# Performance work log

Hardware: AMD Instinct MI355X
Metric: run time of the kernel (lower is better)

## Reference

```python
import jax, jax.numpy as jnp
import numpy as np

IN_CH = 64
NODE = 48
K_NEIGS = 10
KERNEL = 5
STRIDE = 2
BN_EPS = 1e-5


def _local_kernel(size, k, s):
    idx = np.arange(size * size).reshape(size, size)
    win = np.lib.stride_tricks.sliding_window_view(idx, (k, k))[::s, ::s]
    patches = win.reshape(-1, k * k)  # [n_edges, k*k] pixel indices
    n_edges = patches.shape[0]
    H = np.zeros((size * size, n_edges), dtype=np.float32)
    H[patches.reshape(-1), np.repeat(np.arange(n_edges), k * k)] = 1.0
    return jnp.asarray(H)


def _pairwise_distance(x):
    # (B,N,C) -> (B,N,N) squared euclidean
    xsq = jnp.sum(x * x, axis=-1, keepdims=True)
    return xsq - 2.0 * jnp.einsum('bnc,bmc->bnm', x, x) + jnp.swapaxes(xsq, 1, 2)


def _batched_knn(x, k):
    d = _pairwise_distance(x)
    avg = d.mean(-1, keepdims=True)
    neg_vals, inds = jax.lax.top_k(-d, k + 1)  # smallest k+1, sorted ascending
    return -neg_vals, inds, d, avg


def _incidence(inds, N):
    # weights_function(prob=False) == ones; scatter ones then transpose
    B, _, K = inds.shape
    b = jnp.arange(B)[:, None, None]
    p = jnp.arange(N)[None, :, None]
    M = jnp.zeros((B, N, N), dtype=jnp.float32).at[b, p, inds].set(1.0)
    return jnp.swapaxes(M, 1, 2)


def _generate_G(H):
    # G = diag(DV^-0.5) @ H @ I @ diag(DE^-1) @ H^T @ diag(DV^-0.5)
    DV = H.sum(axis=2)  # (B,N)
    DE = H.sum(axis=1)  # (B,E)
    dv2 = DV ** -0.5
    Hs = H * (1.0 / DE)[:, None, :]
    M = jnp.einsum('bne,bme->bnm', Hs, H)
    return dv2[:, :, None] * M * dv2[:, None, :]


def _build_G(x, local_H):
    B, N, C = x.shape
    _, topk_inds, _, _ = _batched_knn(x, K_NEIGS)
    H1 = _incidence(topk_inds, N)
    Dv = H1.sum(axis=2, keepdims=True)  # alpha = 1.0
    max_k = int(jnp.max(Dv))  # data-dependent width (eager, matches torch)
    _, ti2, _, _ = _batched_knn(x, max_k - 1)  # (B,N,max_k)
    tk = jnp.arange(max_k)[None, None, :]
    rng = jnp.broadcast_to(jnp.arange(N)[None, :, None], (B, N, max_k))
    new_inds = jnp.where(tk >= Dv, rng, ti2)
    new_H = _incidence(new_inds, N)
    loc = jnp.broadcast_to(local_H[None], (B,) + local_H.shape)
    return _generate_G(jnp.concatenate([new_H, loc], axis=2))


def _hgnn(x, G, W, b, gamma, beta):
    h = jnp.einsum('bnc,oc->bno', x, W) + b  # Linear
    h = jnp.einsum('bnm,bmc->bnc', G, h)
    mean = h.mean(axis=(0, 1))  # BatchNorm1d over (B,N) per channel
    var = h.var(axis=(0, 1))
    h = gamma * (h - mean) / jnp.sqrt(var + BN_EPS) + beta
    return jax.nn.relu(h) + x


def setup_inputs() -> dict:
    key = jax.random.key(0)
    k1, k2, k3 = jax.random.split(key, 3)
    B, N, C = 4, NODE * NODE, IN_CH
    x = jax.random.normal(k1, (B, N, C), dtype=jnp.float32)
    W = jax.random.normal(k2, (C, C), dtype=jnp.float32) / np.sqrt(C)
    b = jax.random.normal(k3, (C,), dtype=jnp.float32) * 0.01
    gamma = jnp.ones((C,), dtype=jnp.float32)
    beta = jnp.zeros((C,), dtype=jnp.float32)
    return {"x": x, "W": W, "b": b, "gamma": gamma, "beta": beta}


def reference(x, W, b, gamma, beta):
    local_H = _local_kernel(NODE, KERNEL, STRIDE)
    G = _build_G(x, local_H)  # graph construction is no_grad in torch
    return _hgnn(x, G, W, b, gamma, beta)
```

## Files before the change

### kernel.cpp

```cpp
#include <hip/hip_runtime.h>


#define HB    4
#define HN    2304
#define HC    64
#define HK    11
#define HL    48
#define HW    22
#define HE2   484
#define HE    (HN + HE2)
#define HRPB  4
#define NSLOT 36
#define NPAIRS (HB * HK * HN)

__global__ void hg14_sentinel(float* out, int n) {
    int i = blockIdx.x * 256 + threadIdx.x;
    if (i < n) out[i] = 12345.0f;
}

__global__ void hg14_init(int* Dv, int* indeg, float* bnsum, float* bnss) {
    int i = blockIdx.x * 256 + threadIdx.x;
    if (i < HB * HN) { Dv[i] = 0; indeg[i] = 0; }
    if (i < HC) { bnsum[i] = 0.f; bnss[i] = 0.f; }
}

__global__ __launch_bounds__(64) void hg14_linear(const float* x, const float* W,
                                                  const float* bias, float* h1,
                                                  float* xsq, float* xT) {
    int row = blockIdx.x;
    int t = threadIdx.x;
    __shared__ float xr[HC];
    float v = x[row * HC + t];
    xr[t] = v;
    __syncthreads();
    float sq = v * v;
    #pragma unroll
    for (int o = 32; o > 0; o >>= 1) sq += __shfl_xor(sq, o);
    if (t == 0) xsq[row] = sq;
    int b = row / HN, n = row % HN;
    xT[(b * HC + t) * HN + n] = v;
    float acc = bias[t];
    #pragma unroll 8
    for (int c = 0; c < HC; c++) acc += xr[c] * W[t * HC + c];
    h1[row * HC + t] = acc;
}

__device__ __forceinline__ unsigned hg14_wave_min_u32(unsigned v) {
    #pragma unroll
    for (int o = 32; o > 0; o >>= 1) {
        unsigned ov = __shfl_xor(v, o);
        v = ov < v ? ov : v;
    }
    return v;
}

#define HG14_INS4(q0, q1, q2, q3, x)                                     \
    {                                                                    \
        unsigned long long x_ = (x), n_;                                 \
        n_ = q0 < x_ ? q0 : x_; x_ = q0 < x_ ? x_ : q0; q0 = n_;         \
        n_ = q1 < x_ ? q1 : x_; x_ = q1 < x_ ? x_ : q1; q1 = n_;         \
        n_ = q2 < x_ ? q2 : x_; x_ = q2 < x_ ? x_ : q2; q2 = n_;         \
        if (x_ < q3) q3 = x_;                                            \
    }

#define HG14_CE(u, v)                                                    \
    { unsigned long long t_ = u < v ? u : v; v = u < v ? v : u; u = t_; }

#define HG14_BUILD()                                                               \
    {                                                                              \
        unsigned long long a0 = CINF, a1 = CINF, a2 = CINF, a3 = CINF;             \
        unsigned long long b0 = CINF, b1 = CINF, b2 = CINF, b3 = CINF;             \
        _Pragma("unroll")                                                          \
        for (int s = 0; s < NSLOT / 2; s++) {                                      \
            unsigned long long pa = ((unsigned long long)key[s] << 12) |           \
                                    (unsigned)((s << 6) | lane);                   \
            unsigned long long pb = ((unsigned long long)key[s + 18] << 12) |      \
                                    (unsigned)(((s + 18) << 6) | lane);            \
            HG14_INS4(a0, a1, a2, a3, pa);                                         \
            HG14_INS4(b0, b1, b2, b3, pb);                                         \
        }                                                                          \
        c0 = a0 < b3 ? a0 : b3; c1 = a1 < b2 ? a1 : b2;                            \
        c2 = a2 < b1 ? a2 : b1; c3 = a3 < b0 ? a3 : b0;                            \
        HG14_CE(c0, c2); HG14_CE(c1, c3); HG14_CE(c0, c1); HG14_CE(c2, c3);        \
    }

#define HG14_EXTRACT(kk, EMIT)                                                     \
    {                                                                              \
        for (int j = 0; j < (kk); j++) {                                           \
            unsigned hk = (unsigned)(c0 >> 12);                                    \
            unsigned mk = hg14_wave_min_u32(hk);                                   \
            unsigned long long bal = __ballot(hk == mk);                           \
            bool iswin;                                                            \
            if (__popcll(bal) == 1) {                                              \
                iswin = (hk == mk);                                                \
            } else {                                                               \
                unsigned mc = (hk == mk) ? (unsigned)(c0 & 0xFFFu) : 0xFFFFFFFFu;  \
                unsigned mm = hg14_wave_min_u32(mc);                               \
                iswin = (mc == mm);                                                \
            }                                                                      \
            if (iswin) {                                                           \
                int bi = (int)(c0 & 0xFFFu);                                       \
                EMIT;                                                              \
                unsigned long long popped = c0;                                    \
                c0 = c1; c1 = c2; c2 = c3; c3 = CINF;                              \
                if (c0 == CINF) {                                                  \
                    _Pragma("unroll")                                              \
                    for (int s = 0; s < NSLOT; s++) {                              \
                        unsigned long long pk =                                    \
                            ((unsigned long long)key[s] << 12) |                   \
                            (unsigned)((s << 6) | lane);                           \
                        if (pk > popped) HG14_INS4(c0, c1, c2, c3, pk);            \
                    }                                                              \
                }                                                                  \
            }                                                                      \
        }                                                                          \
    }

__device__ __forceinline__ void hg14_kth(const unsigned (&key)[NSLOT], int kk,
                                         unsigned& T, int& cntLess, int& take) {
    unsigned andv = 0xFFFFFFFFu, orv = 0u;
    #pragma unroll
    for (int s = 0; s < NSLOT; s++) { andv &= key[s]; orv |= key[s]; }
    #pragma unroll
    for (int o = 32; o > 0; o >>= 1) {
        andv &= (unsigned)__shfl_xor((int)andv, o);
        orv  |= (unsigned)__shfl_xor((int)orv, o);
    }
    unsigned diff = andv ^ orv;
    if (diff == 0u) { T = andv; cntLess = 0; take = kk; return; }
    int tstart = 31 - __builtin_clz(diff);
    unsigned lowmask = (tstart == 31) ? 0xFFFFFFFFu : ((1u << (tstart + 1)) - 1u);
    unsigned pref = andv & ~lowmask;
    int r = kk;
    for (int t = tstart; t >= 0; t--) {
        unsigned pt = pref >> t;
        int c = 0;
        #pragma unroll
        for (int s = 0; s < NSLOT; s++) c += ((key[s] >> t) == pt) ? 1 : 0;
        #pragma unroll
        for (int o = 32; o > 0; o >>= 1) c += __shfl_xor(c, o);
        if (r > c) { r -= c; pref |= (1u << t); }
    }
    T = pref; cntLess = kk - r; take = r;
}

__device__ __forceinline__ void hg14_scan64(int v, int lane, int& excl, int& total) {
    int inc = v;
    #pragma unroll
    for (int o = 1; o < 64; o <<= 1) {
        int u = __shfl_up(inc, o);
        if (lane >= o) inc += u;
    }
    excl = inc - v;
    total = __shfl(inc, 63);
}

__global__ __launch_bounds__(256) void hg14_knn_count(const float* xT, const float* xsq,
                                                      int* Dv, unsigned int* kcache,
                                                      int storekeys) {
    __shared__ float d[HRPB][HN];
    __shared__ __align__(16) float xrt[HC][HRPB];
    const int t = threadIdx.x;
    const int b = blockIdx.x / (HN / HRPB);
    const int n0 = (blockIdx.x % (HN / HRPB)) * HRPB;
    const int r = t >> 6;
    const int lane = t & 63;
    xrt[lane][r] = xT[(b * HC + lane) * HN + n0 + r];
    __syncthreads();
    float xs[HRPB];
    #pragma unroll
    for (int q = 0; q < HRPB; q++) xs[q] = xsq[b * HN + n0 + q];

    #pragma unroll
    for (int i = 0; i < 4; i++) {
        const int m = 512 * i + 2 * t;
        float2 d0 = {0.f, 0.f}, d1 = {0.f, 0.f}, d2 = {0.f, 0.f}, d3 = {0.f, 0.f};
        #pragma unroll 8
        for (int c = 0; c < HC; c++) {
            float4 xq = *reinterpret_cast<const float4*>(&xrt[c][0]);
            float2 xv = *reinterpret_cast<const float2*>(&xT[(b * HC + c) * HN + m]);
            d0.x += xq.x * xv.x; d0.y += xq.x * xv.y;
            d1.x += xq.y * xv.x; d1.y += xq.y * xv.y;
            d2.x += xq.z * xv.x; d2.y += xq.z * xv.y;
            d3.x += xq.w * xv.x; d3.y += xq.w * xv.y;
        }
        float s0 = xsq[b * HN + m], s1 = xsq[b * HN + m + 1];
        *reinterpret_cast<float2*>(&d[0][m]) =
            make_float2(xs[0] + s0 - 2.f * d0.x, xs[0] + s1 - 2.f * d0.y);
        *reinterpret_cast<float2*>(&d[1][m]) =
            make_float2(xs[1] + s0 - 2.f * d1.x, xs[1] + s1 - 2.f * d1.y);
        *reinterpret_cast<float2*>(&d[2][m]) =
            make_float2(xs[2] + s0 - 2.f * d2.x, xs[2] + s1 - 2.f * d2.y);
        *reinterpret_cast<float2*>(&d[3][m]) =
            make_float2(xs[3] + s0 - 2.f * d3.x, xs[3] + s1 - 2.f * d3.y);
    }
    {
        const int m = 2048 + t;
        float d0 = 0.f, d1 = 0.f, d2 = 0.f, d3 = 0.f;
        #pragma unroll 8
        for (int c = 0; c < HC; c++) {
            float4 xq = *reinterpret_cast<const float4*>(&xrt[c][0]);
            float xv = xT[(b * HC + c) * HN + m];
            d0 += xq.x * xv; d1 += xq.y * xv; d2 += xq.z * xv; d3 += xq.w * xv;
        }
        float sm = xsq[b * HN + m];
        d[0][m] = xs[0] + sm - 2.f * d0;
        d[1][m] = xs[1] + sm - 2.f * d1;
        d[2][m] = xs[2] + sm - 2.f * d2;
        d[3][m] = xs[3] + sm - 2.f * d3;
    }
    __syncthreads();

    const int p = n0 + r;
    const unsigned long long CINF = ~0ull;
    unsigned int key[NSLOT];
    unsigned long long c0, c1, c2, c3;
    const int rowbase = (b * HN + p) * NSLOT;
    #pragma unroll
    for (int s = 0; s < NSLOT; s++) {
        float f = d[r][(s << 6) | lane];
        unsigned int ub = __float_as_uint(f);
        unsigned int k = ub ^ (((unsigned int)(((int)ub) >> 31)) | 0x80000000u);
        key[s] = k;
        if (storekeys) kcache[(rowbase + s) * 64 + lane] = k;
    }
    HG14_BUILD();
    HG14_EXTRACT(HK, atomicAdd(&Dv[b * HN + bi], 1));
}

__global__ __launch_bounds__(256) void hg14_scan(const int* Dv, int* offs) {
    __shared__ int part[256];
    int t = threadIdx.x;
    int base = t * 36;
    int s = 0;
    for (int i = 0; i < 36; i++) s += max(Dv[base + i], 1);
    part[t] = s;
    __syncthreads();
    if (t == 0) { int acc = 0; for (int i = 0; i < 256; i++) { int v = part[i]; part[i] = acc; acc += v; } }
    __syncthreads();
    int acc = part[t];
    for (int i = 0; i < 36; i++) { offs[base + i] = acc; acc += max(Dv[base + i], 1); }
}

__device__ __forceinline__ void hg14_select_emit(const unsigned (&key)[NSLOT],
                                                 int b, int p, int lane, int kk, int base,
                                                 int* indeg, unsigned int* pairs) {
    unsigned T; int cntLess, take;
    hg14_kth(key, kk, T, cntLess, take);
    int cl = 0;
    #pragma unroll
    for (int s = 0; s < NSLOT; s++) cl += (key[s] < T) ? 1 : 0;
    int off, tot;
    hg14_scan64(cl, lane, off, tot);
    int w = 0;
    #pragma unroll
    for (int s = 0; s < NSLOT; s++) {
        if (key[s] < T) {
            int m = (s << 6) | lane;
            atomicAdd(&indeg[b * HN + m], 1);
            pairs[base + off + w] =
                ((unsigned)b << 24) | ((unsigned)p << 12) | (unsigned)m;
            w++;
        }
    }
    int lastm = -1;
    for (int t2 = 0; t2 < take; t2++) {
        int mc = 0x7FFFFFFF;
        #pragma unroll
        for (int s = 0; s < NSLOT; s++) {
            int m = (s << 6) | lane;
            if (key[s] == T && m > lastm && m < mc) mc = m;
        }
        int mmin = mc;
        #pragma unroll
        for (int o = 32; o > 0; o >>= 1) {
            int ov = __shfl_xor(mmin, o);
            mmin = ov < mmin ? ov : mmin;
        }
        if (mc == mmin) {
            atomicAdd(&indeg[b * HN + mmin], 1);
            pairs[base + cntLess + t2] =
                ((unsigned)b << 24) | ((unsigned)p << 12) | (unsigned)mmin;
        }
        lastm = mmin;
    }
}

__global__ __launch_bounds__(256) void hg14_knn_sel_cached(const unsigned int* kcache,
                                                           const int* Dv, const int* offs,
                                                           int* indeg, unsigned int* pairs) {
    const int t = threadIdx.x;
    const int lane = t & 63;
    const int gw = blockIdx.x * HRPB + (t >> 6);
    const int b = gw / HN, p = gw % HN;
    unsigned int key[NSLOT];
    const int rowbase = gw * NSLOT;
    #pragma unroll
    for (int s = 0; s < NSLOT; s++) key[s] = kcache[(rowbase + s) * 64 + lane];
    hg14_select_emit(key, b, p, lane, max(Dv[gw], 1), offs[gw], indeg, pairs);
}

__global__ __launch_bounds__(256) void hg14_knn_sel_full(const float* xT, const float* xsq,
                                                         const int* Dv, const int* offs,
                                                         int* indeg, unsigned int* pairs) {
    __shared__ float d[HRPB][HN];
    __shared__ float xr[HRPB][HC];
    const int t = threadIdx.x;
    const int b = blockIdx.x / (HN / HRPB);
    const int n0 = (blockIdx.x % (HN / HRPB)) * HRPB;
    const int r = t >> 6;
    const int lane = t & 63;
    xr[r][lane] = xT[(b * HC + lane) * HN + n0 + r];
    __syncthreads();
    float xs[HRPB];
    #pragma unroll
    for (int q = 0; q < HRPB; q++) xs[q] = xsq[b * HN + n0 + q];
    for (int m = t; m < HN; m += 256) {
        float dot0 = 0.f, dot1 = 0.f, dot2 = 0.f, dot3 = 0.f;
        #pragma unroll 8
        for (int c = 0; c < HC; c++) {
            float xv = xT[(b * HC + c) * HN + m];
            dot0 += xr[0][c] * xv;
            dot1 += xr[1][c] * xv;
            dot2 += xr[2][c] * xv;
            dot3 += xr[3][c] * xv;
        }
        float xsm = xsq[b * HN + m];
        d[0][m] = xs[0] + xsm - 2.f * dot0;
        d[1][m] = xs[1] + xsm - 2.f * dot1;
        d[2][m] = xs[2] + xsm - 2.f * dot2;
        d[3][m] = xs[3] + xsm - 2.f * dot3;
    }
    __syncthreads();
    const int p = n0 + r;
    unsigned int key[NSLOT];
    #pragma unroll
    for (int s = 0; s < NSLOT; s++) {
        float f = d[r][(s << 6) | lane];
        unsigned int ub = __float_as_uint(f);
        key[s] = ub ^ (((unsigned int)(((int)ub) >> 31)) | 0x80000000u);
    }
    const int gw = b * HN + p;
    hg14_select_emit(key, b, p, lane, max(Dv[gw], 1), offs[gw], indeg, pairs);
}

__device__ __forceinline__ int hg14_lo(int rc) { return max(0, (rc - 3) / 2); }
__device__ __forceinline__ int hg14_hi(int rc) { return min(HW - 1, rc / 2); }

__global__ __launch_bounds__(256) void hg14_scale(float* h1, const int* indeg) {
    int i = blockIdx.x * 256 + threadIdx.x;
    int node = i >> 6;
    int n = node % HN;
    int r = n / HL, c = n % HL;
    int cover = max(0, hg14_hi(r) - hg14_lo(r) + 1) * max(0, hg14_hi(c) - hg14_lo(c) + 1);
    int dvn = max(indeg[node] + cover, 1);
    h1[i] *= rsqrtf((float)dvn);
}

__global__ void hg14_zero(float* z, float* h2) {
    int i = blockIdx.x * 256 + threadIdx.x;
    int b = i / (HN * HC), rem = i % (HN * HC);
    z[b * HE * HC + rem] = 0.f;
    h2[i] = 0.f;
}

__global__ __launch_bounds__(256) void hg14_edge(const unsigned int* pairs, const int* Dv,
                                                 const float* y, float* z) {
    int wv = (blockIdx.x * 256 + threadIdx.x) >> 6;
    int lane = threadIdx.x & 63;
    if (wv < NPAIRS) {
        unsigned int pk = pairs[wv];
        int b = pk >> 24;
        if (b >= HB) return;
        int p = (pk >> 12) & 0xFFF, m = pk & 0xFFF;
        float invde = 1.f / (float)max(Dv[b * HN + p], 1);
        atomicAdd(&z[(b * HE + p) * HC + lane], y[(b * HN + m) * HC + lane] * invde);
    } else {
        int w2 = wv - NPAIRS;
        if (w2 >= HB * HE2) return;
        int b = w2 / HE2, w = w2 % HE2;
        int wr = w / HW, wc = w % HW;
        float acc = 0.f;
        #pragma unroll
        for (int i = 0; i < 5; i++)
            #pragma unroll
            for (int j = 0; j < 5; j++)
                acc += y[(b * HN + (wr * 2 + i) * HL + wc * 2 + j) * HC + lane];
        z[(b * HE + HN + w) * HC + lane] = acc * (1.f / 25.f);
    }
}

__global__ __launch_bounds__(256) void hg14_gscatter(const unsigned int* pairs,
                                                     const float* z, float* h2) {
    int idx = (blockIdx.x * 256 + threadIdx.x) >> 6;
    int lane = threadIdx.x & 63;
    if (idx >= NPAIRS) return;
    unsigned int pk = pairs[idx];
    int b = pk >> 24;
    if (b >= HB) return;
    int p = (pk >> 12) & 0xFFF, m = pk & 0xFFF;
    atomicAdd(&h2[(b * HN + m) * HC + lane], z[(b * HE + p) * HC + lane]);
}

__global__ __launch_bounds__(256) void hg14_gfinish(const float* z, const int* indeg, float* h2) {
    int wave = (blockIdx.x * 256 + threadIdx.x) >> 6;
    int lane = threadIdx.x & 63;
    int b = wave / HN, n = wave % HN;
    int g = b * HN + n;
    float acc = h2[g * HC + lane];
    int r = n / HL, c = n % HL;
    int rlo = hg14_lo(r), rhi = hg14_hi(r), clo = hg14_lo(c), chi = hg14_hi(c);
    for (int wr = rlo; wr <= rhi; wr++)
        for (int wc = clo; wc <= chi; wc++)
            acc += z[(b * HE + HN + wr * HW + wc) * HC + lane];
    int dvn = max(indeg[g] + max(0, rhi - rlo + 1) * max(0, chi - clo + 1), 1);
    h2[g * HC + lane] = acc * rsqrtf((float)dvn);
}

__global__ __launch_bounds__(256) void hg14_bnstats(const float* h2, float* bnsum, float* bnss) {
    int t = threadIdx.x;
    int c = t & 63, rg = t >> 6;
    int row0 = blockIdx.x * 36;
    float s = 0.f, ss = 0.f;
    for (int r = rg; r < 36; r += 4) {
        float v = h2[(row0 + r) * HC + c];
        s += v; ss += v * v;
    }
    __shared__ float ls[256], lss[256];
    ls[t] = s; lss[t] = ss;
    __syncthreads();
    if (t < 64) {
        s  = ls[t]  + ls[t + 64]  + ls[t + 128]  + ls[t + 192];
        ss = lss[t] + lss[t + 64] + lss[t + 128] + lss[t + 192];
        atomicAdd(&bnsum[t], s);
        atomicAdd(&bnss[t], ss);
    }
}

__global__ __launch_bounds__(256) void hg14_final(const float* h2, const float* x,
                                                  const float* gamma, const float* beta,
                                                  const float* bnsum, const float* bnss,
                                                  float* out) {
    int i = blockIdx.x * 256 + threadIdx.x;
    int c = i & 63;
    const float M = (float)(HB * HN);
    float mean = bnsum[c] / M;
    float var  = bnss[c] / M - mean * mean;
    float inv  = rsqrtf(var + 1e-5f);
    float h = gamma[c] * (h2[i] - mean) * inv + beta[c];
    out[i] = fmaxf(h, 0.f) + x[i];
}

extern "C" void kernel_launch(void* const* d_in, const int* in_sizes, int n_in,
                              void* d_out, int out_size, void* d_ws, size_t ws_size,
                              hipStream_t stream) {
    const float* x     = (const float*)d_in[0];
    const float* W     = (const float*)d_in[1];
    const float* bias  = (const float*)d_in[2];
    const float* gamma = (const float*)d_in[3];
    const float* beta  = (const float*)d_in[4];
    float* out = (float*)d_out;
    (void)in_sizes; (void)n_in;

    char* ws = (char*)d_ws;
    size_t off = 0;
    float*        xsq     = (float*)(ws + off);        off += (size_t)HB * HN * 4;
    float*        h1      = (float*)(ws + off);        off += (size_t)HB * HN * HC * 4;
    float*        h2      = (float*)(ws + off);        off += (size_t)HB * HN * HC * 4;
    int*          Dv      = (int*)(ws + off);          off += (size_t)HB * HN * 4;
    int*          indeg   = (int*)(ws + off);          off += (size_t)HB * HN * 4;
    int*          offs    = (int*)(ws + off);          off += (size_t)HB * HN * 4;
    unsigned int* pairs   = (unsigned int*)(ws + off); off += (size_t)NPAIRS * 4;
    float*        bnsum   = (float*)(ws + off);        off += 256;
    float*        bnss    = (float*)(ws + off);        off += 256;
    float*        xT      = (float*)(ws + off);
    float*        z       = (float*)(ws + off);
    off += (size_t)HB * HE * HC * 4;
    size_t base_need = off;
    unsigned int* kcache  = (unsigned int*)(ws + off);
    size_t cache_need = off + (size_t)HB * HN * NSLOT * 64 * 4;

    if (ws_size < base_need) {
        hg14_sentinel<<<(out_size + 255) / 256, 256, 0, stream>>>(out, out_size);
        return;
    }
    const int use_cache = (ws_size >= cache_need) ? 1 : 0;

    const int EDGE_WAVES = NPAIRS + HB * HE2;

    hg14_init<<<(HB * HN + 255) / 256, 256, 0, stream>>>(Dv, indeg, bnsum, bnss);
    hg14_linear<<<HB * HN, 64, 0, stream>>>(x, W, bias, h1, xsq, xT);
    hg14_knn_count<<<HB * (HN / HRPB), 256, 0, stream>>>(xT, xsq, Dv, kcache, use_cache);
    hg14_scan<<<1, 256, 0, stream>>>(Dv, offs);
    if (use_cache)
        hg14_knn_sel_cached<<<HB * (HN / HRPB), 256, 0, stream>>>(kcache, Dv, offs, indeg, pairs);
    else
        hg14_knn_sel_full<<<HB * (HN / HRPB), 256, 0, stream>>>(xT, xsq, Dv, offs, indeg, pairs);
    hg14_scale<<<(HB * HN * HC) / 256, 256, 0, stream>>>(h1, indeg);
    hg14_zero<<<(HB * HN * HC) / 256, 256, 0, stream>>>(z, h2);
    hg14_edge<<<EDGE_WAVES / 4, 256, 0, stream>>>(pairs, Dv, h1, z);
    hg14_gscatter<<<(NPAIRS * 64) / 256, 256, 0, stream>>>(pairs, z, h2);
    hg14_gfinish<<<(HB * HN) / 4, 256, 0, stream>>>(z, indeg, h2);
    hg14_bnstats<<<256, 256, 0, stream>>>(h2, bnsum, bnss);
    hg14_final<<<(HB * HN * HC) / 256, 256, 0, stream>>>(h2, x, gamma, beta, bnsum, bnss, out);
}
```

Before: 377.3 us.

## Replace atomic scatter in hypergraph propagation with CSR gather using reverse index

After: 415.0 us. +10.0%, slower.

```diff
diff --git a/kernel.cpp b/kernel.cpp
--- a/kernel.cpp
+++ b/kernel.cpp
@@ -18,9 +18,9 @@
     if (i < n) out[i] = 12345.0f;
 }
 
-__global__ void hg14_init(int* Dv, int* indeg, float* bnsum, float* bnss) {
+__global__ void hg18_init(int* Dv, int* indeg, int* cursor, float* bnsum, float* bnss) {
     int i = blockIdx.x * 256 + threadIdx.x;
-    if (i < HB * HN) { Dv[i] = 0; indeg[i] = 0; }
+    if (i < HB * HN) { Dv[i] = 0; indeg[i] = 0; cursor[i] = 0; }
     if (i < HC) { bnsum[i] = 0.f; bnss[i] = 0.f; }
 }
 
@@ -228,18 +228,46 @@
     HG14_EXTRACT(HK, atomicAdd(&Dv[b * HN + bi], 1));
 }
 
-__global__ __launch_bounds__(256) void hg14_scan(const int* Dv, int* offs) {
-    __shared__ int part[256];
+__global__ __launch_bounds__(256) void hg15_scan(const int* Dv, int* offs) {
+    __shared__ int wsum[4];
     int t = threadIdx.x;
+    int lane = t & 63, w = t >> 6;
     int base = t * 36;
     int s = 0;
     for (int i = 0; i < 36; i++) s += max(Dv[base + i], 1);
-    part[t] = s;
-    __syncthreads();
-    if (t == 0) { int acc = 0; for (int i = 0; i < 256; i++) { int v = part[i]; part[i] = acc; acc += v; } }
-    __syncthreads();
-    int acc = part[t];
+    int inc = s;
+    #pragma unroll
+    for (int o = 1; o < 64; o <<= 1) {
+        int u = __shfl_up(inc, o);
+        if (lane >= o) inc += u;
+    }
+    if (lane == 63) wsum[w] = inc;
+    __syncthreads();
+    int woff = 0;
+    for (int i = 0; i < w; i++) woff += wsum[i];
+    int acc = woff + inc - s;
     for (int i = 0; i < 36; i++) { offs[base + i] = acc; acc += max(Dv[base + i], 1); }
+}
+
+__global__ __launch_bounds__(256) void hg18_scan2(const int* indeg, int* offs2) {
+    __shared__ int wsum[4];
+    int t = threadIdx.x;
+    int lane = t & 63, w = t >> 6;
+    int base = t * 36;
+    int s = 0;
+    for (int i = 0; i < 36; i++) s += indeg[base + i];
+    int inc = s;
+    #pragma unroll
+    for (int o = 1; o < 64; o <<= 1) {
+        int u = __shfl_up(inc, o);
+        if (lane >= o) inc += u;
+    }
+    if (lane == 63) wsum[w] = inc;
+    __syncthreads();
+    int woff = 0;
+    for (int i = 0; i < w; i++) woff += wsum[i];
+    int acc = woff + inc - s;
+    for (int i = 0; i < 36; i++) { offs2[base + i] = acc; acc += indeg[base + i]; }
 }
 
 __device__ __forceinline__ void hg14_select_emit(const unsigned (&key)[NSLOT],
@@ -344,6 +372,20 @@
     hg14_select_emit(key, b, p, lane, max(Dv[gw], 1), offs[gw], indeg, pairs);
 }
 
+__global__ __launch_bounds__(256) void hg18_revbuild(const unsigned int* pairs,
+                                                     const int* offs2, int* cursor,
+                                                     unsigned int* rev) {
+    int idx = blockIdx.x * 256 + threadIdx.x;
+    if (idx >= NPAIRS) return;
+    unsigned int pk = pairs[idx];
+    int b = pk >> 24;
+    if (b >= HB) return;
+    int p = (pk >> 12) & 0xFFF, m = pk & 0xFFF;
+    int g = b * HN + m;
+    int slot = atomicAdd(&cursor[g], 1);
+    rev[offs2[g] + slot] = (unsigned)p;
+}
+
 __device__ __forceinline__ int hg14_lo(int rc) { return max(0, (rc - 3) / 2); }
 __device__ __forceinline__ int hg14_hi(int rc) { return min(HW - 1, rc / 2); }
 
@@ -357,26 +399,26 @@
     h1[i] *= rsqrtf((float)dvn);
 }
 
-__global__ void hg14_zero(float* z, float* h2) {
-    int i = blockIdx.x * 256 + threadIdx.x;
-    int b = i / (HN * HC), rem = i % (HN * HC);
-    z[b * HE * HC + rem] = 0.f;
-    h2[i] = 0.f;
-}
-
-__global__ __launch_bounds__(256) void hg14_edge(const unsigned int* pairs, const int* Dv,
-                                                 const float* y, float* z) {
+__global__ __launch_bounds__(256) void hg18_edge_gather(const unsigned int* pairs,
+                                                        const int* Dv, const int* offs,
+                                                        const float* y, float* z) {
     int wv = (blockIdx.x * 256 + threadIdx.x) >> 6;
     int lane = threadIdx.x & 63;
-    if (wv < NPAIRS) {
-        unsigned int pk = pairs[wv];
-        int b = pk >> 24;
-        if (b >= HB) return;
-        int p = (pk >> 12) & 0xFFF, m = pk & 0xFFF;
-        float invde = 1.f / (float)max(Dv[b * HN + p], 1);
-        atomicAdd(&z[(b * HE + p) * HC + lane], y[(b * HN + m) * HC + lane] * invde);
+    if (wv < HB * HN) {
+        int b = wv / HN, p = wv % HN;
+        int g = b * HN + p;
+        int kk = max(Dv[g], 1);
+        int base = offs[g];
+        float invde = 1.f / (float)kk;
+        float acc = 0.f;
+        for (int j = 0; j < kk; j++) {
+            unsigned int pk = pairs[base + j];
+            int m = pk & 0xFFF;
+            acc += y[(b * HN + m) * HC + lane] * invde;
+        }
+        z[(b * HE + p) * HC + lane] = acc;
     } else {
-        int w2 = wv - NPAIRS;
+        int w2 = wv - HB * HN;
         if (w2 >= HB * HE2) return;
         int b = w2 / HE2, w = w2 % HE2;
         int wr = w / HW, wc = w % HW;
@@ -390,30 +432,26 @@
     }
 }
 
-__global__ __launch_bounds__(256) void hg14_gscatter(const unsigned int* pairs,
-                                                     const float* z, float* h2) {
-    int idx = (blockIdx.x * 256 + threadIdx.x) >> 6;
-    int lane = threadIdx.x & 63;
-    if (idx >= NPAIRS) return;
-    unsigned int pk = pairs[idx];
-    int b = pk >> 24;
-    if (b >= HB) return;
-    int p = (pk >> 12) & 0xFFF, m = pk & 0xFFF;
-    atomicAdd(&h2[(b * HN + m) * HC + lane], z[(b * HE + p) * HC + lane]);
-}
-
-__global__ __launch_bounds__(256) void hg14_gfinish(const float* z, const int* indeg, float* h2) {
+__global__ __launch_bounds__(256) void hg18_gfinish2(const float* z, const int* indeg,
+                                                     const int* offs2, const unsigned int* rev,
+                                                     float* h2) {
     int wave = (blockIdx.x * 256 + threadIdx.x) >> 6;
     int lane = threadIdx.x & 63;
     int b = wave / HN, n = wave % HN;
     int g = b * HN + n;
-    float acc = h2[g * HC + lane];
+    float acc = 0.f;
+    int deg = indeg[g];
+    int base2 = offs2[g];
+    for (int j = 0; j < deg; j++) {
+        int p = (int)rev[base2 + j];
+        acc += z[(b * HE + p) * HC + lane];
+    }
     int r = n / HL, c = n % HL;
     int rlo = hg14_lo(r), rhi = hg14_hi(r), clo = hg14_lo(c), chi = hg14_hi(c);
     for (int wr = rlo; wr <= rhi; wr++)
         for (int wc = clo; wc <= chi; wc++)
             acc += z[(b * HE + HN + wr * HW + wc) * HC + lane];
-    int dvn = max(indeg[g] + max(0, rhi - rlo + 1) * max(0, chi - clo + 1), 1);
+    int dvn = max(deg + max(0, rhi - rlo + 1) * max(0, chi - clo + 1), 1);
     h2[g * HC + lane] = acc * rsqrtf((float)dvn);
 }
 
@@ -470,7 +508,10 @@
     int*          Dv      = (int*)(ws + off);          off += (size_t)HB * HN * 4;
     int*          indeg   = (int*)(ws + off);          off += (size_t)HB * HN * 4;
     int*          offs    = (int*)(ws + off);          off += (size_t)HB * HN * 4;
+    int*          offs2   = (int*)(ws + off);          off += (size_t)HB * HN * 4;
+    int*          cursor  = (int*)(ws + off);          off += (size_t)HB * HN * 4;
     unsigned int* pairs   = (unsigned int*)(ws + off); off += (size_t)NPAIRS * 4;
+    unsigned int* rev     = (unsigned int*)(ws + off); off += (size_t)NPAIRS * 4;
     float*        bnsum   = (float*)(ws + off);        off += 256;
     float*        bnss    = (float*)(ws + off);        off += 256;
     float*        xT      = (float*)(ws + off);
@@ -486,21 +527,21 @@
     }
     const int use_cache = (ws_size >= cache_need) ? 1 : 0;
 
-    const int EDGE_WAVES = NPAIRS + HB * HE2;
-
-    hg14_init<<<(HB * HN + 255) / 256, 256, 0, stream>>>(Dv, indeg, bnsum, bnss);
+    const int EDGE_WAVES = HB * HN + HB * HE2;
+
+    hg18_init<<<(HB * HN + 255) / 256, 256, 0, stream>>>(Dv, indeg, cursor, bnsum, bnss);
     hg14_linear<<<HB * HN, 64, 0, stream>>>(x, W, bias, h1, xsq, xT);
     hg14_knn_count<<<HB * (HN / HRPB), 256, 0, stream>>>(xT, xsq, Dv, kcache, use_cache);
-    hg14_scan<<<1, 256, 0, stream>>>(Dv, offs);
+    hg15_scan<<<1, 256, 0, stream>>>(Dv, offs);
     if (use_cache)
         hg14_knn_sel_cached<<<HB * (HN / HRPB), 256, 0, stream>>>(kcache, Dv, offs, indeg, pairs);
     else
         hg14_knn_sel_full<<<HB * (HN / HRPB), 256, 0, stream>>>(xT, xsq, Dv, offs, indeg, pairs);
+    hg18_scan2<<<1, 256, 0, stream>>>(indeg, offs2);
+    hg18_revbuild<<<(NPAIRS + 255) / 256, 256, 0, stream>>>(pairs, offs2, cursor, rev);
     hg14_scale<<<(HB * HN * HC) / 256, 256, 0, stream>>>(h1, indeg);
-    hg14_zero<<<(HB * HN * HC) / 256, 256, 0, stream>>>(z, h2);
-    hg14_edge<<<EDGE_WAVES / 4, 256, 0, stream>>>(pairs, Dv, h1, z);
-    hg14_gscatter<<<(NPAIRS * 64) / 256, 256, 0, stream>>>(pairs, z, h2);
-    hg14_gfinish<<<(HB * HN) / 4, 256, 0, stream>>>(z, indeg, h2);
+    hg18_edge_gather<<<EDGE_WAVES / 4, 256, 0, stream>>>(pairs, Dv, offs, h1, z);
+    hg18_gfinish2<<<(HB * HN) / 4, 256, 0, stream>>>(z, indeg, offs2, rev, h2);
     hg14_bnstats<<<256, 256, 0, stream>>>(h2, bnsum, bnss);
     hg14_final<<<(HB * HN * HC) / 256, 256, 0, stream>>>(h2, x, gamma, beta, bnsum, bnss, out);
 }
```

## Cache sorted top-64 candidates in kNN count and select from them

Applied to the files above, without the earlier changes.

Measured after the change: 403.6 us. 1.07x slower.

```diff
diff --git a/kernel.cpp b/kernel.cpp
--- a/kernel.cpp
+++ b/kernel.cpp
@@ -11,6 +11,7 @@
 #define HE    (HN + HE2)
 #define HRPB  4
 #define NSLOT 36
+#define NCAND 64
 #define NPAIRS (HB * HK * HN)
 
 __global__ void hg14_sentinel(float* out, int n) {
@@ -44,77 +45,6 @@
     for (int c = 0; c < HC; c++) acc += xr[c] * W[t * HC + c];
     h1[row * HC + t] = acc;
 }
-
-__device__ __forceinline__ unsigned hg14_wave_min_u32(unsigned v) {
-    #pragma unroll
-    for (int o = 32; o > 0; o >>= 1) {
-        unsigned ov = __shfl_xor(v, o);
-        v = ov < v ? ov : v;
-    }
-    return v;
-}
-
-#define HG14_INS4(q0, q1, q2, q3, x)                                     \
-    {                                                                    \
-        unsigned long long x_ = (x), n_;                                 \
-        n_ = q0 < x_ ? q0 : x_; x_ = q0 < x_ ? x_ : q0; q0 = n_;         \
-        n_ = q1 < x_ ? q1 : x_; x_ = q1 < x_ ? x_ : q1; q1 = n_;         \
-        n_ = q2 < x_ ? q2 : x_; x_ = q2 < x_ ? x_ : q2; q2 = n_;         \
-        if (x_ < q3) q3 = x_;                                            \
-    }
-
-#define HG14_CE(u, v)                                                    \
-    { unsigned long long t_ = u < v ? u : v; v = u < v ? v : u; u = t_; }
-
-#define HG14_BUILD()                                                               \
-    {                                                                              \
-        unsigned long long a0 = CINF, a1 = CINF, a2 = CINF, a3 = CINF;             \
-        unsigned long long b0 = CINF, b1 = CINF, b2 = CINF, b3 = CINF;             \
-        _Pragma("unroll")                                                          \
-        for (int s = 0; s < NSLOT / 2; s++) {                                      \
-            unsigned long long pa = ((unsigned long long)key[s] << 12) |           \
-                                    (unsigned)((s << 6) | lane);                   \
-            unsigned long long pb = ((unsigned long long)key[s + 18] << 12) |      \
-                                    (unsigned)(((s + 18) << 6) | lane);            \
-            HG14_INS4(a0, a1, a2, a3, pa);                                         \
-            HG14_INS4(b0, b1, b2, b3, pb);                                         \
-        }                                                                          \
-        c0 = a0 < b3 ? a0 : b3; c1 = a1 < b2 ? a1 : b2;                            \
-        c2 = a2 < b1 ? a2 : b1; c3 = a3 < b0 ? a3 : b0;                            \
-        HG14_CE(c0, c2); HG14_CE(c1, c3); HG14_CE(c0, c1); HG14_CE(c2, c3);        \
-    }
-
-#define HG14_EXTRACT(kk, EMIT)                                                     \
-    {                                                                              \
-        for (int j = 0; j < (kk); j++) {                                           \
-            unsigned hk = (unsigned)(c0 >> 12);                                    \
-            unsigned mk = hg14_wave_min_u32(hk);                                   \
-            unsigned long long bal = __ballot(hk == mk);                           \
-            bool iswin;                                                            \
-            if (__popcll(bal) == 1) {                                              \
-                iswin = (hk == mk);                                                \
-            } else {                                                               \
-                unsigned mc = (hk == mk) ? (unsigned)(c0 & 0xFFFu) : 0xFFFFFFFFu;  \
-                unsigned mm = hg14_wave_min_u32(mc);                               \
-                iswin = (mc == mm);                                                \
-            }                                                                      \
-            if (iswin) {                                                           \
-                int bi = (int)(c0 & 0xFFFu);                                       \
-                EMIT;                                                              \
-                unsigned long long popped = c0;                                    \
-                c0 = c1; c1 = c2; c2 = c3; c3 = CINF;                              \
-                if (c0 == CINF) {                                                  \
-                    _Pragma("unroll")                                              \
-                    for (int s = 0; s < NSLOT; s++) {                              \
-                        unsigned long long pk =                                    \
-                            ((unsigned long long)key[s] << 12) |                   \
-                            (unsigned)((s << 6) | lane);                           \
-                        if (pk > popped) HG14_INS4(c0, c1, c2, c3, pk);            \
-                    }                                                              \
-                }                                                                  \
-            }                                                                      \
-        }                                                                          \
-    }
 
 __device__ __forceinline__ void hg14_kth(const unsigned (&key)[NSLOT], int kk,
                                          unsigned& T, int& cntLess, int& take) {
@@ -155,10 +85,9 @@
     total = __shfl(inc, 63);
 }
 
-__global__ __launch_bounds__(256) void hg14_knn_count(const float* xT, const float* xsq,
-                                                      int* Dv, unsigned int* kcache,
-                                                      int storekeys) {
-    __shared__ float d[HRPB][HN];
+__global__ __launch_bounds__(256) void hg19_knn_count(const float* xT, const float* xsq,
+                                                      int* Dv, unsigned short* ccache) {
+    __shared__ __align__(16) float d[HRPB][HN];
     __shared__ __align__(16) float xrt[HC][HRPB];
     const int t = threadIdx.x;
     const int b = blockIdx.x / (HN / HRPB);
@@ -212,34 +141,100 @@
     __syncthreads();
 
     const int p = n0 + r;
-    const unsigned long long CINF = ~0ull;
     unsigned int key[NSLOT];
-    unsigned long long c0, c1, c2, c3;
-    const int rowbase = (b * HN + p) * NSLOT;
     #pragma unroll
     for (int s = 0; s < NSLOT; s++) {
         float f = d[r][(s << 6) | lane];
         unsigned int ub = __float_as_uint(f);
-        unsigned int k = ub ^ (((unsigned int)(((int)ub) >> 31)) | 0x80000000u);
-        key[s] = k;
-        if (storekeys) kcache[(rowbase + s) * 64 + lane] = k;
-    }
-    HG14_BUILD();
-    HG14_EXTRACT(HK, atomicAdd(&Dv[b * HN + bi], 1));
-}
-
-__global__ __launch_bounds__(256) void hg14_scan(const int* Dv, int* offs) {
-    __shared__ int part[256];
+        key[s] = ub ^ (((unsigned int)(((int)ub) >> 31)) | 0x80000000u);
+    }
+
+    unsigned T; int cntLess, take;
+    hg14_kth(key, NCAND, T, cntLess, take);
+    unsigned long long* scr = reinterpret_cast<unsigned long long*>(&d[r][0]);
+    int cl = 0;
+    #pragma unroll
+    for (int s = 0; s < NSLOT; s++) cl += (key[s] < T) ? 1 : 0;
+    int off, tot;
+    hg14_scan64(cl, lane, off, tot);
+    int w = 0;
+    #pragma unroll
+    for (int s = 0; s < NSLOT; s++) {
+        if (key[s] < T) {
+            int m = (s << 6) | lane;
+            scr[off + w] = ((unsigned long long)key[s] << 12) | (unsigned)m;
+            w++;
+        }
+    }
+    int lastm = -1;
+    for (int t2 = 0; t2 < take; t2++) {
+        int mc = 0x7FFFFFFF;
+        #pragma unroll
+        for (int s = 0; s < NSLOT; s++) {
+            int m = (s << 6) | lane;
+            if (key[s] == T && m > lastm && m < mc) mc = m;
+        }
+        int mmin = mc;
+        #pragma unroll
+        for (int o = 32; o > 0; o >>= 1) {
+            int ov = __shfl_xor(mmin, o);
+            mmin = ov < mmin ? ov : mmin;
+        }
+        if (mc == mmin) scr[cntLess + t2] = ((unsigned long long)T << 12) | (unsigned)mmin;
+        lastm = mmin;
+    }
+    unsigned long long v = scr[lane];
+    #pragma unroll
+    for (int k = 2; k <= 64; k <<= 1) {
+        #pragma unroll
+        for (int j = k >> 1; j > 0; j >>= 1) {
+            unsigned long long o = __shfl_xor(v, j);
+            bool takeMin = (((lane & k) == 0) == ((lane & j) == 0));
+            unsigned long long mn = v < o ? v : o;
+            unsigned long long mx = v < o ? o : v;
+            v = takeMin ? mn : mx;
+        }
+    }
+    int m = (int)(v & 0xFFFu);
+    if (lane < HK) atomicAdd(&Dv[b * HN + m], 1);
+    ccache[(size_t)(b * HN + p) * NCAND + lane] = (unsigned short)m;
+}
+
+__global__ __launch_bounds__(256) void hg15_scan(const int* Dv, int* offs) {
+    __shared__ int wsum[4];
     int t = threadIdx.x;
+    int lane = t & 63, w = t >> 6;
     int base = t * 36;
     int s = 0;
     for (int i = 0; i < 36; i++) s += max(Dv[base + i], 1);
-    part[t] = s;
-    __syncthreads();
-    if (t == 0) { int acc = 0; for (int i = 0; i < 256; i++) { int v = part[i]; part[i] = acc; acc += v; } }
-    __syncthreads();
-    int acc = part[t];
+    int inc = s;
+    #pragma unroll
+    for (int o = 1; o < 64; o <<= 1) {
+        int u = __shfl_up(inc, o);
+        if (lane >= o) inc += u;
+    }
+    if (lane == 63) wsum[w] = inc;
+    __syncthreads();
+    int woff = 0;
+    for (int i = 0; i < w; i++) woff += wsum[i];
+    int acc = woff + inc - s;
     for (int i = 0; i < 36; i++) { offs[base + i] = acc; acc += max(Dv[base + i], 1); }
+}
+
+__global__ __launch_bounds__(256) void hg19_sel(const unsigned short* ccache,
+                                                const int* Dv, const int* offs,
+                                                int* indeg, unsigned int* pairs) {
+    const int t = threadIdx.x;
+    const int lane = t & 63;
+    const int gw = blockIdx.x * HRPB + (t >> 6);
+    const int b = gw / HN, p = gw % HN;
+    int kk = max(Dv[gw], 1);
+    if (kk <= NCAND && lane < kk) {
+        int m = ccache[(size_t)gw * NCAND + lane];
+        atomicAdd(&indeg[b * HN + m], 1);
+        pairs[offs[gw] + lane] =
+            ((unsigned)b << 24) | ((unsigned)p << 12) | (unsigned)m;
+    }
 }
 
 __device__ __forceinline__ void hg14_select_emit(const unsigned (&key)[NSLOT],
@@ -286,28 +281,18 @@
     }
 }
 
-__global__ __launch_bounds__(256) void hg14_knn_sel_cached(const unsigned int* kcache,
-                                                           const int* Dv, const int* offs,
-                                                           int* indeg, unsigned int* pairs) {
-    const int t = threadIdx.x;
-    const int lane = t & 63;
-    const int gw = blockIdx.x * HRPB + (t >> 6);
-    const int b = gw / HN, p = gw % HN;
-    unsigned int key[NSLOT];
-    const int rowbase = gw * NSLOT;
-    #pragma unroll
-    for (int s = 0; s < NSLOT; s++) key[s] = kcache[(rowbase + s) * 64 + lane];
-    hg14_select_emit(key, b, p, lane, max(Dv[gw], 1), offs[gw], indeg, pairs);
-}
-
-__global__ __launch_bounds__(256) void hg14_knn_sel_full(const float* xT, const float* xsq,
+__global__ __launch_bounds__(256) void hg19_sel_fallback(const float* xT, const float* xsq,
                                                          const int* Dv, const int* offs,
                                                          int* indeg, unsigned int* pairs) {
-    __shared__ float d[HRPB][HN];
-    __shared__ float xr[HRPB][HC];
     const int t = threadIdx.x;
     const int b = blockIdx.x / (HN / HRPB);
     const int n0 = (blockIdx.x % (HN / HRPB)) * HRPB;
+    bool need = false;
+    #pragma unroll
+    for (int q = 0; q < HRPB; q++) need |= (Dv[b * HN + n0 + q] > NCAND);
+    if (!need) return;
+    __shared__ float d[HRPB][HN];
+    __shared__ float xr[HRPB][HC];
     const int r = t >> 6;
     const int lane = t & 63;
     xr[r][lane] = xT[(b * HC + lane) * HN + n0 + r];
@@ -333,6 +318,9 @@
     }
     __syncthreads();
     const int p = n0 + r;
+    const int gw = b * HN + p;
+    int kk = max(Dv[gw], 1);
+    if (kk <= NCAND) return;
     unsigned int key[NSLOT];
     #pragma unroll
     for (int s = 0; s < NSLOT; s++) {
@@ -340,8 +328,7 @@
         unsigned int ub = __float_as_uint(f);
         key[s] = ub ^ (((unsigned int)(((int)ub) >> 31)) | 0x80000000u);
     }
-    const int gw = b * HN + p;
-    hg14_select_emit(key, b, p, lane, max(Dv[gw], 1), offs[gw], indeg, pairs);
+    hg14_select_emit(key, b, p, lane, kk, offs[gw], indeg, pairs);
 }
 
 __device__ __forceinline__ int hg14_lo(int rc) { return max(0, (rc - 3) / 2); }
@@ -464,38 +451,34 @@
 
     char* ws = (char*)d_ws;
     size_t off = 0;
-    float*        xsq     = (float*)(ws + off);        off += (size_t)HB * HN * 4;
-    float*        h1      = (float*)(ws + off);        off += (size_t)HB * HN * HC * 4;
-    float*        h2      = (float*)(ws + off);        off += (size_t)HB * HN * HC * 4;
-    int*          Dv      = (int*)(ws + off);          off += (size_t)HB * HN * 4;
-    int*          indeg   = (int*)(ws + off);          off += (size_t)HB * HN * 4;
-    int*          offs    = (int*)(ws + off);          off += (size_t)HB * HN * 4;
-    unsigned int* pairs   = (unsigned int*)(ws + off); off += (size_t)NPAIRS * 4;
-    float*        bnsum   = (float*)(ws + off);        off += 256;
-    float*        bnss    = (float*)(ws + off);        off += 256;
-    float*        xT      = (float*)(ws + off);
-    float*        z       = (float*)(ws + off);
+    float*          xsq     = (float*)(ws + off);          off += (size_t)HB * HN * 4;
+    float*          h1      = (float*)(ws + off);          off += (size_t)HB * HN * HC * 4;
+    float*          h2      = (float*)(ws + off);          off += (size_t)HB * HN * HC * 4;
+    int*            Dv      = (int*)(ws + off);            off += (size_t)HB * HN * 4;
+    int*            indeg   = (int*)(ws + off);            off += (size_t)HB * HN * 4;
+    int*            offs    = (int*)(ws + off);            off += (size_t)HB * HN * 4;
+    unsigned int*   pairs   = (unsigned int*)(ws + off);   off += (size_t)NPAIRS * 4;
+    unsigned short* ccache  = (unsigned short*)(ws + off); off += (size_t)HB * HN * NCAND * 2;
+    float*          bnsum   = (float*)(ws + off);          off += 256;
+    float*          bnss    = (float*)(ws + off);          off += 256;
+    float*          xT      = (float*)(ws + off);
+    float*          z       = (float*)(ws + off);
     off += (size_t)HB * HE * HC * 4;
     size_t base_need = off;
-    unsigned int* kcache  = (unsigned int*)(ws + off);
-    size_t cache_need = off + (size_t)HB * HN * NSLOT * 64 * 4;
 
     if (ws_size < base_need) {
         hg14_sentinel<<<(out_size + 255) / 256, 256, 0, stream>>>(out, out_size);
         return;
     }
-    const int use_cache = (ws_size >= cache_need) ? 1 : 0;
 
     const int EDGE_WAVES = NPAIRS + HB * HE2;
 
     hg14_init<<<(HB * HN + 255) / 256, 256, 0, stream>>>(Dv, indeg, bnsum, bnss);
     hg14_linear<<<HB * HN, 64, 0, stream>>>(x, W, bias, h1, xsq, xT);
-    hg14_knn_count<<<HB * (HN / HRPB), 256, 0, stream>>>(xT, xsq, Dv, kcache, use_cache);
-    hg14_scan<<<1, 256, 0, stream>>>(Dv, offs);
-    if (use_cache)
-        hg14_knn_sel_cached<<<HB * (HN / HRPB), 256, 0, stream>>>(kcache, Dv, offs, indeg, pairs);
-    else
-        hg14_knn_sel_full<<<HB * (HN / HRPB), 256, 0, stream>>>(xT, xsq, Dv, offs, indeg, pairs);
+    hg19_knn_count<<<HB * (HN / HRPB), 256, 0, stream>>>(xT, xsq, Dv, ccache);
+    hg15_scan<<<1, 256, 0, stream>>>(Dv, offs);
+    hg19_sel<<<HB * (HN / HRPB), 256, 0, stream>>>(ccache, Dv, offs, indeg, pairs);
+    hg19_sel_fallback<<<HB * (HN / HRPB), 256, 0, stream>>>(xT, xsq, Dv, offs, indeg, pairs);
     hg14_scale<<<(HB * HN * HC) / 256, 256, 0, stream>>>(h1, indeg);
     hg14_zero<<<(HB * HN * HC) / 256, 256, 0, stream>>>(z, h2);
     hg14_edge<<<EDGE_WAVES / 4, 256, 0, stream>>>(pairs, Dv, h1, z);
```

## Cache sorted top-48 neighbor indices instead of full distance keys for selection

Applied to the files above, without the earlier changes.

Result: slower. 410.5 us (+8.8%).

```diff
diff --git a/kernel.cpp b/kernel.cpp
--- a/kernel.cpp
+++ b/kernel.cpp
@@ -11,6 +11,7 @@
 #define HE    (HN + HE2)
 #define HRPB  4
 #define NSLOT 36
+#define NCAND 48
 #define NPAIRS (HB * HK * HN)
 
 __global__ void hg14_sentinel(float* out, int n) {
@@ -155,9 +156,8 @@
     total = __shfl(inc, 63);
 }
 
-__global__ __launch_bounds__(256) void hg14_knn_count(const float* xT, const float* xsq,
-                                                      int* Dv, unsigned int* kcache,
-                                                      int storekeys) {
+__global__ __launch_bounds__(256) void hg20_knn_count(const float* xT, const float* xsq,
+                                                      int* Dv, unsigned short* ccache) {
     __shared__ float d[HRPB][HN];
     __shared__ __align__(16) float xrt[HC][HRPB];
     const int t = threadIdx.x;
@@ -215,31 +215,54 @@
     const unsigned long long CINF = ~0ull;
     unsigned int key[NSLOT];
     unsigned long long c0, c1, c2, c3;
-    const int rowbase = (b * HN + p) * NSLOT;
+    const size_t rowc = (size_t)(b * HN + p) * NCAND;
     #pragma unroll
     for (int s = 0; s < NSLOT; s++) {
         float f = d[r][(s << 6) | lane];
         unsigned int ub = __float_as_uint(f);
-        unsigned int k = ub ^ (((unsigned int)(((int)ub) >> 31)) | 0x80000000u);
-        key[s] = k;
-        if (storekeys) kcache[(rowbase + s) * 64 + lane] = k;
+        key[s] = ub ^ (((unsigned int)(((int)ub) >> 31)) | 0x80000000u);
     }
     HG14_BUILD();
-    HG14_EXTRACT(HK, atomicAdd(&Dv[b * HN + bi], 1));
-}
-
-__global__ __launch_bounds__(256) void hg14_scan(const int* Dv, int* offs) {
-    __shared__ int part[256];
+    HG14_EXTRACT(NCAND,
+        { if (j < HK) atomicAdd(&Dv[b * HN + bi], 1);
+          ccache[rowc + j] = (unsigned short)bi; });
+}
+
+__global__ __launch_bounds__(256) void hg15_scan(const int* Dv, int* offs) {
+    __shared__ int wsum[4];
     int t = threadIdx.x;
+    int lane = t & 63, w = t >> 6;
     int base = t * 36;
     int s = 0;
     for (int i = 0; i < 36; i++) s += max(Dv[base + i], 1);
-    part[t] = s;
-    __syncthreads();
-    if (t == 0) { int acc = 0; for (int i = 0; i < 256; i++) { int v = part[i]; part[i] = acc; acc += v; } }
-    __syncthreads();
-    int acc = part[t];
+    int inc = s;
+    #pragma unroll
+    for (int o = 1; o < 64; o <<= 1) {
+        int u = __shfl_up(inc, o);
+        if (lane >= o) inc += u;
+    }
+    if (lane == 63) wsum[w] = inc;
+    __syncthreads();
+    int woff = 0;
+    for (int i = 0; i < w; i++) woff += wsum[i];
+    int acc = woff + inc - s;
     for (int i = 0; i < 36; i++) { offs[base + i] = acc; acc += max(Dv[base + i], 1); }
+}
+
+__global__ __launch_bounds__(256) void hg19_sel(const unsigned short* ccache,
+                                                const int* Dv, const int* offs,
+                                                int* indeg, unsigned int* pairs) {
+    const int t = threadIdx.x;
+    const int lane = t & 63;
+    const int gw = blockIdx.x * HRPB + (t >> 6);
+    const int b = gw / HN, p = gw % HN;
+    int kk = max(Dv[gw], 1);
+    if (kk <= NCAND && lane < kk) {
+        int m = ccache[(size_t)gw * NCAND + lane];
+        atomicAdd(&indeg[b * HN + m], 1);
+        pairs[offs[gw] + lane] =
+            ((unsigned)b << 24) | ((unsigned)p << 12) | (unsigned)m;
+    }
 }
 
 __device__ __forceinline__ void hg14_select_emit(const unsigned (&key)[NSLOT],
@@ -286,28 +309,18 @@
     }
 }
 
-__global__ __launch_bounds__(256) void hg14_knn_sel_cached(const unsigned int* kcache,
-                                                           const int* Dv, const int* offs,
-                                                           int* indeg, unsigned int* pairs) {
-    const int t = threadIdx.x;
-    const int lane = t & 63;
-    const int gw = blockIdx.x * HRPB + (t >> 6);
-    const int b = gw / HN, p = gw % HN;
-    unsigned int key[NSLOT];
-    const int rowbase = gw * NSLOT;
-    #pragma unroll
-    for (int s = 0; s < NSLOT; s++) key[s] = kcache[(rowbase + s) * 64 + lane];
-    hg14_select_emit(key, b, p, lane, max(Dv[gw], 1), offs[gw], indeg, pairs);
-}
-
-__global__ __launch_bounds__(256) void hg14_knn_sel_full(const float* xT, const float* xsq,
+__global__ __launch_bounds__(256) void hg19_sel_fallback(const float* xT, const float* xsq,
                                                          const int* Dv, const int* offs,
                                                          int* indeg, unsigned int* pairs) {
-    __shared__ float d[HRPB][HN];
-    __shared__ float xr[HRPB][HC];
     const int t = threadIdx.x;
     const int b = blockIdx.x / (HN / HRPB);
     const int n0 = (blockIdx.x % (HN / HRPB)) * HRPB;
+    bool need = false;
+    #pragma unroll
+    for (int q = 0; q < HRPB; q++) need |= (Dv[b * HN + n0 + q] > NCAND);
+    if (!need) return;
+    __shared__ float d[HRPB][HN];
+    __shared__ float xr[HRPB][HC];
     const int r = t >> 6;
     const int lane = t & 63;
     xr[r][lane] = xT[(b * HC + lane) * HN + n0 + r];
@@ -333,6 +346,9 @@
     }
     __syncthreads();
     const int p = n0 + r;
+    const int gw = b * HN + p;
+    int kk = max(Dv[gw], 1);
+    if (kk <= NCAND) return;
     unsigned int key[NSLOT];
     #pragma unroll
     for (int s = 0; s < NSLOT; s++) {
@@ -340,8 +356,7 @@
         unsigned int ub = __float_as_uint(f);
         key[s] = ub ^ (((unsigned int)(((int)ub) >> 31)) | 0x80000000u);
     }
-    const int gw = b * HN + p;
-    hg14_select_emit(key, b, p, lane, max(Dv[gw], 1), offs[gw], indeg, pairs);
+    hg14_select_emit(key, b, p, lane, kk, offs[gw], indeg, pairs);
 }
 
 __device__ __forceinline__ int hg14_lo(int rc) { return max(0, (rc - 3) / 2); }
@@ -464,38 +479,34 @@
 
     char* ws = (char*)d_ws;
     size_t off = 0;
-    float*        xsq     = (float*)(ws + off);        off += (size_t)HB * HN * 4;
-    float*        h1      = (float*)(ws + off);        off += (size_t)HB * HN * HC * 4;
-    float*        h2      = (float*)(ws + off);        off += (size_t)HB * HN * HC * 4;
-    int*          Dv      = (int*)(ws + off);          off += (size_t)HB * HN * 4;
-    int*          indeg   = (int*)(ws + off);          off += (size_t)HB * HN * 4;
-    int*          offs    = (int*)(ws + off);          off += (size_t)HB * HN * 4;
-    unsigned int* pairs   = (unsigned int*)(ws + off); off += (size_t)NPAIRS * 4;
-    float*        bnsum   = (float*)(ws + off);        off += 256;
-    float*        bnss    = (float*)(ws + off);        off += 256;
-    float*        xT      = (float*)(ws + off);
-    float*        z       = (float*)(ws + off);
+    float*          xsq     = (float*)(ws + off);          off += (size_t)HB * HN * 4;
+    float*          h1      = (float*)(ws + off);          off += (size_t)HB * HN * HC * 4;
+    float*          h2      = (float*)(ws + off);          off += (size_t)HB * HN * HC * 4;
+    int*            Dv      = (int*)(ws + off);            off += (size_t)HB * HN * 4;
+    int*            indeg   = (int*)(ws + off);            off += (size_t)HB * HN * 4;
+    int*            offs    = (int*)(ws + off);            off += (size_t)HB * HN * 4;
+    unsigned int*   pairs   = (unsigned int*)(ws + off);   off += (size_t)NPAIRS * 4;
+    unsigned short* ccache  = (unsigned short*)(ws + off); off += (size_t)HB * HN * NCAND * 2;
+    float*          bnsum   = (float*)(ws + off);          off += 256;
+    float*          bnss    = (float*)(ws + off);          off += 256;
+    float*          xT      = (float*)(ws + off);
+    float*          z       = (float*)(ws + off);
     off += (size_t)HB * HE * HC * 4;
     size_t base_need = off;
-    unsigned int* kcache  = (unsigned int*)(ws + off);
-    size_t cache_need = off + (size_t)HB * HN * NSLOT * 64 * 4;
 
     if (ws_size < base_need) {
         hg14_sentinel<<<(out_size + 255) / 256, 256, 0, stream>>>(out, out_size);
         return;
     }
-    const int use_cache = (ws_size >= cache_need) ? 1 : 0;
 
     const int EDGE_WAVES = NPAIRS + HB * HE2;
 
     hg14_init<<<(HB * HN + 255) / 256, 256, 0, stream>>>(Dv, indeg, bnsum, bnss);
     hg14_linear<<<HB * HN, 64, 0, stream>>>(x, W, bias, h1, xsq, xT);
-    hg14_knn_count<<<HB * (HN / HRPB), 256, 0, stream>>>(xT, xsq, Dv, kcache, use_cache);
-    hg14_scan<<<1, 256, 0, stream>>>(Dv, offs);
-    if (use_cache)
-        hg14_knn_sel_cached<<<HB * (HN / HRPB), 256, 0, stream>>>(kcache, Dv, offs, indeg, pairs);
-    else
-        hg14_knn_sel_full<<<HB * (HN / HRPB), 256, 0, stream>>>(xT, xsq, Dv, offs, indeg, pairs);
+    hg20_knn_count<<<HB * (HN / HRPB), 256, 0, stream>>>(xT, xsq, Dv, ccache);
+    hg15_scan<<<1, 256, 0, stream>>>(Dv, offs);
+    hg19_sel<<<HB * (HN / HRPB), 256, 0, stream>>>(ccache, Dv, offs, indeg, pairs);
+    hg19_sel_fallback<<<HB * (HN / HRPB), 256, 0, stream>>>(xT, xsq, Dv, offs, indeg, pairs);
     hg14_scale<<<(HB * HN * HC) / 256, 256, 0, stream>>>(h1, indeg);
     hg14_zero<<<(HB * HN * HC) / 256, 256, 0, stream>>>(z, h2);
     hg14_edge<<<EDGE_WAVES / 4, 256, 0, stream>>>(pairs, Dv, h1, z);
```
